# Kernel optimization log

Measured on AMD Instinct MI355X. Metric: run time of the kernel, lower is better.

The kernel has to match this reference:

```python
import jax, jax.numpy as jnp
import numpy as np

D, H, DK, L, F, V = 512, 16, 32, 16, 1024, 32768
C1, C2, CORE, LG, MD, B = 512, 256, 256, 64, 64, 16
T_IN = C1 + C2 + CORE      # 1024
T_TF = CORE + LG + MD      # 384


def _ln(x, g, b, eps=1e-5):
    mu = x.mean(-1, keepdims=True)
    var = ((x - mu) ** 2).mean(-1, keepdims=True)
    return (x - mu) * jax.lax.rsqrt(var + eps) * g + b


def _heads(x):  # [B,T,D] -> [B,H,T,DK]
    b, t, _ = x.shape
    return x.reshape(b, t, H, DK).transpose(0, 2, 1, 3)


def _summarizer(ids, sem, pos, inw, inb, outw, outb, tok, lng, lnb):
    b, t = ids.shape
    x = sem[ids] + pos[:t][None]                      # [B,T,D]
    wq, wk, wv = jnp.split(inw, 3, axis=0)
    bq, bk, bv = jnp.split(inb, 3, axis=0)
    q = _heads(jnp.broadcast_to(tok, (b, tok.shape[1], D)) @ wq.T + bq)
    k = _heads(x @ wk.T + bk)
    v = _heads(x @ wv.T + bv)
    s = jnp.einsum('bhqd,bhkd->bhqk', q, k) / jnp.sqrt(jnp.float32(DK))
    a = jax.nn.softmax(s, axis=-1)
    o = jnp.einsum('bhqk,bhkd->bhqd', a, v).transpose(0, 2, 1, 3).reshape(b, -1, D)
    return _ln(o @ outw.T + outb, lng, lnb)


def _forward(emb_sem, emb_pos,
             lg_sem, lg_pos, lg_inw, lg_inb, lg_outw, lg_outb, lg_tok, lg_lng, lg_lnb,
             md_sem, md_pos, md_inw, md_inb, md_outw, md_outb, md_tok, md_lng, md_lnb,
             qkv_w, qkv_b, wo_w, wo_b, ln1_g, ln1_b, ln2_g, ln2_b,
             ff1_w, ff1_b, ff2_w, ff2_b, hd_lng, hd_lnb, hd_w, hd_b,
             input_ids, target_ids):
    lg_ids = input_ids[:, -(C1 + C2 + CORE):-(C2 + CORE)]
    md_ids = input_ids[:, -(C2 + CORE):-CORE]
    core_ids = input_ids[:, -CORE:]
    tgt = target_ids[:, -CORE:]

    lg_emb = _summarizer(lg_ids, lg_sem, lg_pos, lg_inw, lg_inb, lg_outw, lg_outb, lg_tok, lg_lng, lg_lnb)
    md_emb = _summarizer(md_ids, md_sem, md_pos, md_inw, md_inb, md_outw, md_outb, md_tok, md_lng, md_lnb)
    x_core = emb_sem[core_ids] + emb_pos[:CORE][None]
    x = jnp.concatenate([lg_emb, md_emb, x_core], axis=1)   # [B, 384, D]

    mask = jnp.tril(jnp.ones((T_TF, T_TF), dtype=bool))

    def step(x, p):
        qw, qb, ow, ob, g1, b1, g2, b2, f1w, f1b, f2w, f2b = p
        h = _ln(x, g1, b1)
        qkv = h @ qw.T + qb
        q, k, v = (_heads(t) for t in jnp.split(qkv, 3, axis=-1))
        s = jnp.einsum('bhqd,bhkd->bhqk', q, k) / jnp.sqrt(jnp.float32(DK))
        s = jnp.where(mask, s, -jnp.inf)
        a = jax.nn.softmax(s, axis=-1)
        o = jnp.einsum('bhqk,bhkd->bhqd', a, v).transpose(0, 2, 1, 3).reshape(x.shape)
        x = x + o @ ow.T + ob
        h2 = _ln(x, g2, b2)
        ff = jax.nn.gelu(h2 @ f1w.T + f1b, approximate=False) @ f2w.T + f2b
        return x + ff, None

    x, _ = jax.lax.scan(step, x, (qkv_w, qkv_b, wo_w, wo_b, ln1_g, ln1_b,
                                  ln2_g, ln2_b, ff1_w, ff1_b, ff2_w, ff2_b))
    logits = (_ln(x, hd_lng, hd_lnb) @ hd_w.T + hd_b)[:, -CORE:, :]
    return logits, tgt


def setup_inputs() -> dict:
    key = jax.random.key(0)
    ks = jax.random.split(key, 24)
    def rn(k, shape, s=0.02):
        return jax.random.normal(k, shape, jnp.float32) * s
    z, o = jnp.zeros, jnp.ones
    return {
        'input_ids': jax.random.randint(ks[0], (B, T_IN), 0, V),
        'target_ids': jax.random.randint(ks[1], (B, T_IN), 0, V),
        'emb_sem': rn(ks[2], (V, D)), 'emb_pos': rn(ks[3], (CORE, D)),
        'lg_sem': rn(ks[4], (V, D)), 'lg_pos': rn(ks[5], (C1, D)),
        'lg_inw': rn(ks[6], (3 * D, D)), 'lg_inb': z(3 * D),
        'lg_outw': rn(ks[7], (D, D)), 'lg_outb': z(D),
        'lg_tok': rn(ks[8], (1, LG, D), 1.0), 'lg_lng': o(D), 'lg_lnb': z(D),
        'md_sem': rn(ks[9], (V, D)), 'md_pos': rn(ks[10], (C2, D)),
        'md_inw': rn(ks[11], (3 * D, D)), 'md_inb': z(3 * D),
        'md_outw': rn(ks[12], (D, D)), 'md_outb': z(D),
        'md_tok': rn(ks[13], (1, MD, D), 1.0), 'md_lng': o(D), 'md_lnb': z(D),
        'qkv_w': rn(ks[14], (L, 3 * D, D)), 'qkv_b': z((L, 3 * D)),
        'wo_w': rn(ks[15], (L, D, D)), 'wo_b': z((L, D)),
        'ln1_g': o((L, D)), 'ln1_b': z((L, D)), 'ln2_g': o((L, D)), 'ln2_b': z((L, D)),
        'ff1_w': rn(ks[16], (L, F, D)), 'ff1_b': z((L, F)),
        'ff2_w': rn(ks[17], (L, D, F)), 'ff2_b': z((L, D)),
        'hd_lng': o(D), 'hd_lnb': z(D), 'hd_w': rn(ks[18], (V, D)), 'hd_b': z(V),
    }


def reference(input_ids, target_ids, emb_sem, emb_pos,
              lg_sem, lg_pos, lg_inw, lg_inb, lg_outw, lg_outb, lg_tok, lg_lng, lg_lnb,
              md_sem, md_pos, md_inw, md_inb, md_outw, md_outb, md_tok, md_lng, md_lnb,
              qkv_w, qkv_b, wo_w, wo_b, ln1_g, ln1_b, ln2_g, ln2_b,
              ff1_w, ff1_b, ff2_w, ff2_b, hd_lng, hd_lnb, hd_w, hd_b):
    return _forward(emb_sem, emb_pos,
                    lg_sem, lg_pos, lg_inw, lg_inb, lg_outw, lg_outb, lg_tok, lg_lng, lg_lnb,
                    md_sem, md_pos, md_inw, md_inb, md_outw, md_outb, md_tok, md_lng, md_lnb,
                    qkv_w, qkv_b, wo_w, wo_b, ln1_g, ln1_b, ln2_g, ln2_b,
                    ff1_w, ff1_b, ff2_w, ff2_b, hd_lng, hd_lnb, hd_w, hd_b,
                    input_ids, target_ids)
```

## Files before the change

### kernel.cpp

```cpp
#include <hip/hip_runtime.h>
#include <hip/hip_bf16.h>
#include <math.h>

#define D 512
#define NHEAD 16
#define DK 32
#define NLAYER 16
#define FF 1024
#define VOC 32768
#define TTF 384
#define NCORE 256
#define NB 16

typedef __attribute__((ext_vector_type(8))) short bfrag;
typedef __attribute__((ext_vector_type(4))) float f32x4;

typedef __attribute__((address_space(3))) void lds_void;
typedef const __attribute__((address_space(1))) void gbl_void;
__device__ __forceinline__ void gload16(const void* g, void* l) {
    __builtin_amdgcn_global_load_lds((gbl_void*)g, (lds_void*)l, 16, 0, 0);
}

__device__ __forceinline__ float gelu_f(float v) {
    return 0.5f * v * (1.0f + erff(v * 0.70710678118654752f));
}

__device__ __forceinline__ void bf8_to_f32(uint4 u, float* v) {
    const __hip_bfloat16* t = reinterpret_cast<const __hip_bfloat16*>(&u);
    #pragma unroll
    for (int e = 0; e < 8; e++) v[e] = __bfloat162float(t[e]);
}
__device__ __forceinline__ uint4 f32_to_bf8(const float* v) {
    uint4 u; __hip_bfloat16* t = reinterpret_cast<__hip_bfloat16*>(&u);
    #pragma unroll
    for (int e = 0; e < 8; e++) t[e] = __float2bfloat16(v[e]);
    return u;
}

__global__ __launch_bounds__(256) void cvt_k(const float* __restrict__ in,
                                             __hip_bfloat16* __restrict__ out, int n)
{
    int i = (blockIdx.x * 256 + threadIdx.x) * 8;
    if (i >= n) return;
    float v[8];
    float4 a = *reinterpret_cast<const float4*>(in + i);
    float4 b = *reinterpret_cast<const float4*>(in + i + 4);
    v[0]=a.x; v[1]=a.y; v[2]=a.z; v[3]=a.w; v[4]=b.x; v[5]=b.y; v[6]=b.z; v[7]=b.w;
    *reinterpret_cast<uint4*>(out + i) = f32_to_bf8(v);
}

__global__ __launch_bounds__(256) void cvtpad_k(const float* __restrict__ in,
                                                __hip_bfloat16* __restrict__ out, int n, int ntot)
{
    int i = (blockIdx.x * 256 + threadIdx.x) * 8;
    if (i >= ntot) return;
    float v[8] = {0.f,0.f,0.f,0.f,0.f,0.f,0.f,0.f};
    if (i < n) {
        float4 a = *reinterpret_cast<const float4*>(in + i);
        float4 b = *reinterpret_cast<const float4*>(in + i + 4);
        v[0]=a.x; v[1]=a.y; v[2]=a.z; v[3]=a.w; v[4]=b.x; v[5]=b.y; v[6]=b.z; v[7]=b.w;
    }
    *reinterpret_cast<uint4*>(out + i) = f32_to_bf8(v);
}

__global__ __launch_bounds__(128) void embed_k(
    const int* __restrict__ ids, int id_stride, int id_off,
    const float* __restrict__ sem, const float* __restrict__ pos,
    __hip_bfloat16* __restrict__ out, int out_stride, int out_off)
{
    int t = blockIdx.x, b = blockIdx.y, tid = threadIdx.x;
    int id = ids[b * id_stride + id_off + t];
    const float4* s4 = reinterpret_cast<const float4*>(sem + (size_t)id * D);
    const float4* p4 = reinterpret_cast<const float4*>(pos + (size_t)t * D);
    size_t row = (size_t)(b * out_stride + out_off + t) * D;
    float4 a = s4[tid], p = p4[tid];
    __hip_bfloat16* o = out + row + tid * 4;
    o[0] = __float2bfloat16(a.x + p.x); o[1] = __float2bfloat16(a.y + p.y);
    o[2] = __float2bfloat16(a.z + p.z); o[3] = __float2bfloat16(a.w + p.w);
}

__global__ __launch_bounds__(256) void mgemm_k(
    const __hip_bfloat16* __restrict__ A, const __hip_bfloat16* __restrict__ W,
    const float* __restrict__ bias, void* __restrict__ C,
    int M, int N, int K, int flags, int order, int RT)
{
    __shared__ __align__(16) __hip_bfloat16 sA[2][8192];
    __shared__ __align__(16) __hip_bfloat16 sB[2][8192];
    int tid = threadIdx.x;
    int w = tid >> 6, lane = tid & 63;
    int wr = w >> 1, wc = w & 1;

    int nbx = gridDim.x, nby = gridDim.y;
    int nwg = nbx * nby;
    int bid0 = blockIdx.y * nbx + blockIdx.x;
    int bid = bid0;
    if (nwg >= 8) {
        int q = nwg >> 3, r = nwg & 7;
        int xcd = bid0 & 7, lb = bid0 >> 3;
        bid = (xcd < r ? xcd * (q + 1) : r * (q + 1) + (xcd - r) * q) + lb;
    }
    int bx, byg;
    if (order == 1) { bx = bid / nby; byg = bid - bx * nby; }
    else            { byg = bid / nbx; bx = bid - byg * nbx; }
    int col0 = bx * 128;

    int srow = lane >> 3;
    int scg  = (lane & 7) ^ srow;
    int cr = lane >> 4;
    int cc = lane & 15;

    const __hip_bfloat16* gB[4];
    #pragma unroll
    for (int r = 0; r < 4; r++) {
        int blk = r * 4 + w;
        gB[r] = W + (size_t)(col0 + blk * 8 + srow) * K + scg * 8;
    }

    for (int t = 0; t < RT; t++) {
        int row0 = (byg * RT + t) * 128;

        const __hip_bfloat16* gA[4];
        #pragma unroll
        for (int r = 0; r < 4; r++) {
            int blk = r * 4 + w;
            gA[r] = A + (size_t)(row0 + blk * 8 + srow) * K + scg * 8;
        }

        f32x4 acc[4][4];
        #pragma unroll
        for (int m = 0; m < 4; m++)
            #pragma unroll
            for (int n = 0; n < 4; n++) acc[m][n] = (f32x4){0.f, 0.f, 0.f, 0.f};

        auto stage = [&](int buf, int k0) {
            #pragma unroll
            for (int r = 0; r < 4; r++) {
                int blk = r * 4 + w;
                gload16(gA[r] + k0, &sA[buf][blk * 512]);
                gload16(gB[r] + k0, &sB[buf][blk * 512]);
            }
        };

        stage(0, 0);
        for (int k0 = 0; k0 < K; k0 += 64) {
            int p = (k0 >> 6) & 1;
            bool more = (k0 + 64 < K);
            if (more) {
                stage(p ^ 1, k0 + 64);
                asm volatile("s_waitcnt vmcnt(8)" ::: "memory");
            } else {
                asm volatile("s_waitcnt vmcnt(0)" ::: "memory");
            }
            __builtin_amdgcn_sched_barrier(0);
            __builtin_amdgcn_s_barrier();
            __builtin_amdgcn_sched_barrier(0);

            #pragma unroll
            for (int ks = 0; ks < 2; ks++) {
                bfrag af[4], bf[4];
                #pragma unroll
                for (int m = 0; m < 4; m++) {
                    int blk = wr * 8 + m * 2 + (cc >> 3);
                    int slot = (ks * 4 + cr) ^ (cc & 7);
                    af[m] = *reinterpret_cast<const bfrag*>(&sA[p][blk * 512 + (cc & 7) * 64 + slot * 8]);
                }
                #pragma unroll
                for (int n = 0; n < 4; n++) {
                    int blk = wc * 8 + n * 2 + (cc >> 3);
                    int slot = (ks * 4 + cr) ^ (cc & 7);
                    bf[n] = *reinterpret_cast<const bfrag*>(&sB[p][blk * 512 + (cc & 7) * 64 + slot * 8]);
                }
                #pragma unroll
                for (int m = 0; m < 4; m++)
                    #pragma unroll
                    for (int n = 0; n < 4; n++)
                        acc[m][n] = __builtin_amdgcn_mfma_f32_16x16x32_bf16(af[m], bf[n], acc[m][n], 0, 0, 0);
            }
            __builtin_amdgcn_sched_barrier(0);
            __builtin_amdgcn_s_barrier();
            __builtin_amdgcn_sched_barrier(0);
        }

        #pragma unroll
        for (int m = 0; m < 4; m++) {
            int rg = row0 + wr * 64 + m * 16 + cr * 4;
            #pragma unroll
            for (int n = 0; n < 4; n++) {
                int cg = col0 + wc * 64 + n * 16 + cc;
                float bs = bias[cg];
                #pragma unroll
                for (int j = 0; j < 4; j++) {
                    float v = acc[m][n][j] + bs;
                    size_t off = (size_t)(rg + j) * N + cg;
                    if (flags == 2)      ((__hip_bfloat16*)C)[off] = __float2bfloat16(gelu_f(v));
                    else if (flags == 3) ((__hip_bfloat16*)C)[off] = __float2bfloat16(v);
                    else                 ((float*)C)[off] = v;
                }
            }
        }
        if (t + 1 < RT) {
            __builtin_amdgcn_s_barrier();
        }
    }
}

template<int IB, int OB>
__global__ __launch_bounds__(256) void ln_k(
    const void* __restrict__ in, void* __restrict__ out,
    const float* __restrict__ g, const float* __restrict__ bt,
    int rpb, int in_stride, int in_off, int out_stride, int out_off)
{
    int r = blockIdx.x * 4 + (threadIdx.x >> 6);
    int b = r / rpb, t = r % rpb;
    size_t irow = (size_t)(b * in_stride + in_off + t) * D;
    size_t orow = (size_t)(b * out_stride + out_off + t) * D;
    int c0 = (threadIdx.x & 63) * 8;
    float v[8];
    if (IB) {
        bf8_to_f32(*reinterpret_cast<const uint4*>((const __hip_bfloat16*)in + irow + c0), v);
    } else {
        float4 a = *reinterpret_cast<const float4*>((const float*)in + irow + c0);
        float4 bq = *reinterpret_cast<const float4*>((const float*)in + irow + c0 + 4);
        v[0]=a.x; v[1]=a.y; v[2]=a.z; v[3]=a.w; v[4]=bq.x; v[5]=bq.y; v[6]=bq.z; v[7]=bq.w;
    }
    float s = 0.f;
    #pragma unroll
    for (int e = 0; e < 8; e++) s += v[e];
    #pragma unroll
    for (int off = 32; off; off >>= 1) s += __shfl_xor(s, off);
    float mu = s * (1.f / 512.f);
    float vs = 0.f;
    #pragma unroll
    for (int e = 0; e < 8; e++) { float d = v[e] - mu; vs += d * d; }
    #pragma unroll
    for (int off = 32; off; off >>= 1) vs += __shfl_xor(vs, off);
    float rstd = rsqrtf(vs * (1.f / 512.f) + 1e-5f);
    float y[8];
    #pragma unroll
    for (int e = 0; e < 8; e++) y[e] = (v[e] - mu) * rstd * g[c0 + e] + bt[c0 + e];
    if (OB) {
        *reinterpret_cast<uint4*>((__hip_bfloat16*)out + orow + c0) = f32_to_bf8(y);
    } else {
        *reinterpret_cast<float4*>((float*)out + orow + c0)     = make_float4(y[0], y[1], y[2], y[3]);
        *reinterpret_cast<float4*>((float*)out + orow + c0 + 4) = make_float4(y[4], y[5], y[6], y[7]);
    }
}

template<int WRITE_H>
__global__ __launch_bounds__(256) void res_ln_k(
    const __hip_bfloat16* __restrict__ delta, __hip_bfloat16* __restrict__ x,
    const float* __restrict__ g, const float* __restrict__ bt,
    __hip_bfloat16* __restrict__ h)
{
    int r = blockIdx.x * 4 + (threadIdx.x >> 6);
    int c0 = (threadIdx.x & 63) * 8;
    size_t row = (size_t)r * D + c0;
    float v[8], dv[8];
    bf8_to_f32(*reinterpret_cast<const uint4*>(x + row), v);
    bf8_to_f32(*reinterpret_cast<const uint4*>(delta + row), dv);
    #pragma unroll
    for (int e = 0; e < 8; e++) v[e] += dv[e];
    *reinterpret_cast<uint4*>(x + row) = f32_to_bf8(v);
    if (WRITE_H) {
        float s = 0.f;
        #pragma unroll
        for (int e = 0; e < 8; e++) s += v[e];
        #pragma unroll
        for (int off = 32; off; off >>= 1) s += __shfl_xor(s, off);
        float mu = s * (1.f / 512.f);
        float vs = 0.f;
        #pragma unroll
        for (int e = 0; e < 8; e++) { float d = v[e] - mu; vs += d * d; }
        #pragma unroll
        for (int off = 32; off; off >>= 1) vs += __shfl_xor(vs, off);
        float rstd = rsqrtf(vs * (1.f / 512.f) + 1e-5f);
        float y[8];
        #pragma unroll
        for (int e = 0; e < 8; e++) y[e] = (v[e] - mu) * rstd * g[c0 + e] + bt[c0 + e];
        *reinterpret_cast<uint4*>(h + row) = f32_to_bf8(y);
    }
}

__global__ __launch_bounds__(512) void fattn_k(
    const __hip_bfloat16* __restrict__ qkv, __hip_bfloat16* __restrict__ o)
{
    __shared__ __align__(16) __hip_bfloat16 Kl[24 * 512];
    __shared__ __align__(16) __hip_bfloat16 Vl[24 * 512];
    __shared__ __align__(16) __hip_bfloat16 Pl[8 * 512];
    int h = blockIdx.x, b = blockIdx.y;
    int tid = threadIdx.x, w = tid >> 6, l = tid & 63;
    const size_t base = (size_t)b * TTF * 1536 + h * DK;

    for (int it = 0; it < 3; it++) {
        int item = it * 512 + tid;
        int key = item >> 2, dg = item & 3;
        uint4 k4 = *reinterpret_cast<const uint4*>(qkv + base + (size_t)key * 1536 + 512 + dg * 8);
        *reinterpret_cast<uint4*>(&Kl[((key >> 4) * 64 + dg * 16 + (key & 15)) * 8]) = k4;
        uint4 v4 = *reinterpret_cast<const uint4*>(qkv + base + (size_t)key * 1536 + 1024 + dg * 8);
        const ushort* ve = reinterpret_cast<const ushort*>(&v4);
        #pragma unroll
        for (int e = 0; e < 8; e++) {
            int dk = dg * 8 + e;
            int f = (((key & 31) >> 3) << 4) | (dk & 15);
            int idx = (((key >> 5) << 1) + (dk >> 4)) * 512 + f * 8 + (key & 7);
            reinterpret_cast<ushort*>(Vl)[idx] = ve[e];
        }
    }
    __syncthreads();

    const float sc = 0.17677669529663687f;
    __hip_bfloat16* pw = Pl + w * 512;

    for (int iq = 0; iq < 3; iq++) {
        int qt = (iq == 0) ? w : (iq == 1 ? 15 - w : 16 + w);
        int q0 = qt * 16;
        bfrag qf = *reinterpret_cast<const bfrag*>(qkv + base + (size_t)(q0 + (l & 15)) * 1536 + (l >> 4) * 8);
        f32x4 oa0 = (f32x4){0.f, 0.f, 0.f, 0.f};
        f32x4 oa1 = (f32x4){0.f, 0.f, 0.f, 0.f};
        float mrun[4], lrun[4];
        #pragma unroll
        for (int jj = 0; jj < 4; jj++) { mrun[jj] = -3.0e38f; lrun[jj] = 0.f; }
        int ksmax = (q0 + 15) >> 5;

        for (int ks = 0; ks <= ksmax; ks++) {
            bfrag kf0 = *reinterpret_cast<const bfrag*>(&Kl[(ks * 2 + 0) * 512 + l * 8]);
            bfrag kf1 = *reinterpret_cast<const bfrag*>(&Kl[(ks * 2 + 1) * 512 + l * 8]);
            f32x4 z = (f32x4){0.f, 0.f, 0.f, 0.f};
            f32x4 s0 = __builtin_amdgcn_mfma_f32_16x16x32_bf16(qf, kf0, z, 0, 0, 0);
            f32x4 s1 = __builtin_amdgcn_mfma_f32_16x16x32_bf16(qf, kf1, z, 0, 0, 0);
            if (ks == ksmax) {
                #pragma unroll
                for (int jj = 0; jj < 4; jj++) {
                    int q = q0 + ((l >> 4) << 2) + jj;
                    if (ks * 32 + (l & 15) > q)      s0[jj] = -3.0e38f;
                    if (ks * 32 + 16 + (l & 15) > q) s1[jj] = -3.0e38f;
                }
            }
            float p0[4], p1[4], ps[4];
            #pragma unroll
            for (int jj = 0; jj < 4; jj++) {
                float sm = fmaxf(s0[jj], s1[jj]);
                #pragma unroll
                for (int off = 1; off <= 8; off <<= 1) sm = fmaxf(sm, __shfl_xor(sm, off));
                float mnew = fmaxf(mrun[jj], sm);
                float f = __expf((mrun[jj] - mnew) * sc);
                mrun[jj] = mnew;
                lrun[jj] *= f;
                oa0[jj] *= f; oa1[jj] *= f;
                p0[jj] = __expf((s0[jj] - mnew) * sc);
                p1[jj] = __expf((s1[jj] - mnew) * sc);
                ps[jj] = p0[jj] + p1[jj];
            }
            #pragma unroll
            for (int jj = 0; jj < 4; jj++) {
                float t = ps[jj];
                #pragma unroll
                for (int off = 1; off <= 8; off <<= 1) t += __shfl_xor(t, off);
                lrun[jj] += t;
            }
            #pragma unroll
            for (int jj = 0; jj < 4; jj++) {
                int ql = ((l >> 4) << 2) + jj;
                int kl0 = l & 15, kl1 = 16 + (l & 15);
                pw[((kl0 >> 3) * 16 + ql) * 8 + (kl0 & 7)] = __float2bfloat16(p0[jj]);
                pw[((kl1 >> 3) * 16 + ql) * 8 + (kl1 & 7)] = __float2bfloat16(p1[jj]);
            }
            bfrag pf  = *reinterpret_cast<const bfrag*>(&pw[l * 8]);
            bfrag vf0 = *reinterpret_cast<const bfrag*>(&Vl[(ks * 2 + 0) * 512 + l * 8]);
            bfrag vf1 = *reinterpret_cast<const bfrag*>(&Vl[(ks * 2 + 1) * 512 + l * 8]);
            oa0 = __builtin_amdgcn_mfma_f32_16x16x32_bf16(pf, vf0, oa0, 0, 0, 0);
            oa1 = __builtin_amdgcn_mfma_f32_16x16x32_bf16(pf, vf1, oa1, 0, 0, 0);
        }
        #pragma unroll
        for (int jj = 0; jj < 4; jj++) {
            float inv = 1.0f / lrun[jj];
            int q = q0 + ((l >> 4) << 2) + jj;
            size_t orow = ((size_t)b * TTF + q) * D + h * DK;
            o[orow + (l & 15)]      = __float2bfloat16(oa0[jj] * inv);
            o[orow + 16 + (l & 15)] = __float2bfloat16(oa1[jj] * inv);
        }
    }
}

template<int TLEN>
__global__ __launch_bounds__(256) void sattn_k(
    const __hip_bfloat16* __restrict__ q, const __hip_bfloat16* __restrict__ kv,
    __hip_bfloat16* __restrict__ o)
{
    __shared__ __align__(16) __hip_bfloat16 Kl[(TLEN / 16) * 512];
    __shared__ __align__(16) __hip_bfloat16 Vl[(TLEN / 16) * 512];
    __shared__ __align__(16) __hip_bfloat16 Pl[4 * 512];
    int h = blockIdx.x, b = blockIdx.y;
    int tid = threadIdx.x, w = tid >> 6, l = tid & 63;

    for (int it = 0; it < TLEN / 64; it++) {
        int item = it * 256 + tid;
        int key = item >> 2, dg = item & 3;
        const __hip_bfloat16* kr = kv + (size_t)(b * TLEN + key) * 1024 + h * DK + dg * 8;
        uint4 k4 = *reinterpret_cast<const uint4*>(kr);
        *reinterpret_cast<uint4*>(&Kl[((key >> 4) * 64 + dg * 16 + (key & 15)) * 8]) = k4;
        uint4 v4 = *reinterpret_cast<const uint4*>(kr + 512);
        const ushort* ve = reinterpret_cast<const ushort*>(&v4);
        #pragma unroll
        for (int e = 0; e < 8; e++) {
            int dk = dg * 8 + e;
            int f = (((key & 31) >> 3) << 4) | (dk & 15);
            int idx = (((key >> 5) << 1) + (dk >> 4)) * 512 + f * 8 + (key & 7);
            reinterpret_cast<ushort*>(Vl)[idx] = ve[e];
        }
    }
    __syncthreads();

    const float sc = 0.17677669529663687f;
    __hip_bfloat16* pw = Pl + w * 512;
    int q0 = w * 16;
    bfrag qf = *reinterpret_cast<const bfrag*>(q + (size_t)(q0 + (l & 15)) * D + h * DK + (l >> 4) * 8);
    f32x4 oa0 = (f32x4){0.f, 0.f, 0.f, 0.f};
    f32x4 oa1 = (f32x4){0.f, 0.f, 0.f, 0.f};
    float mrun[4], lrun[4];
    #pragma unroll
    for (int jj = 0; jj < 4; jj++) { mrun[jj] = -3.0e38f; lrun[jj] = 0.f; }

    for (int ks = 0; ks < TLEN / 32; ks++) {
        bfrag kf0 = *reinterpret_cast<const bfrag*>(&Kl[(ks * 2 + 0) * 512 + l * 8]);
        bfrag kf1 = *reinterpret_cast<const bfrag*>(&Kl[(ks * 2 + 1) * 512 + l * 8]);
        f32x4 z = (f32x4){0.f, 0.f, 0.f, 0.f};
        f32x4 s0 = __builtin_amdgcn_mfma_f32_16x16x32_bf16(qf, kf0, z, 0, 0, 0);
        f32x4 s1 = __builtin_amdgcn_mfma_f32_16x16x32_bf16(qf, kf1, z, 0, 0, 0);
        float p0[4], p1[4], ps[4];
        #pragma unroll
        for (int jj = 0; jj < 4; jj++) {
            float sm = fmaxf(s0[jj], s1[jj]);
            #pragma unroll
            for (int off = 1; off <= 8; off <<= 1) sm = fmaxf(sm, __shfl_xor(sm, off));
            float mnew = fmaxf(mrun[jj], sm);
            float f = __expf((mrun[jj] - mnew) * sc);
            mrun[jj] = mnew;
            lrun[jj] *= f;
            oa0[jj] *= f; oa1[jj] *= f;
            p0[jj] = __expf((s0[jj] - mnew) * sc);
            p1[jj] = __expf((s1[jj] - mnew) * sc);
            ps[jj] = p0[jj] + p1[jj];
        }
        #pragma unroll
        for (int jj = 0; jj < 4; jj++) {
            float t = ps[jj];
            #pragma unroll
            for (int off = 1; off <= 8; off <<= 1) t += __shfl_xor(t, off);
            lrun[jj] += t;
        }
        #pragma unroll
        for (int jj = 0; jj < 4; jj++) {
            int ql = ((l >> 4) << 2) + jj;
            int kl0 = l & 15, kl1 = 16 + (l & 15);
            pw[((kl0 >> 3) * 16 + ql) * 8 + (kl0 & 7)] = __float2bfloat16(p0[jj]);
            pw[((kl1 >> 3) * 16 + ql) * 8 + (kl1 & 7)] = __float2bfloat16(p1[jj]);
        }
        bfrag pf  = *reinterpret_cast<const bfrag*>(&pw[l * 8]);
        bfrag vf0 = *reinterpret_cast<const bfrag*>(&Vl[(ks * 2 + 0) * 512 + l * 8]);
        bfrag vf1 = *reinterpret_cast<const bfrag*>(&Vl[(ks * 2 + 1) * 512 + l * 8]);
        oa0 = __builtin_amdgcn_mfma_f32_16x16x32_bf16(pf, vf0, oa0, 0, 0, 0);
        oa1 = __builtin_amdgcn_mfma_f32_16x16x32_bf16(pf, vf1, oa1, 0, 0, 0);
    }
    #pragma unroll
    for (int jj = 0; jj < 4; jj++) {
        float inv = 1.0f / lrun[jj];
        int qi = q0 + ((l >> 4) << 2) + jj;
        size_t orow = ((size_t)b * 64 + qi) * D + h * DK;
        o[orow + (l & 15)]      = __float2bfloat16(oa0[jj] * inv);
        o[orow + 16 + (l & 15)] = __float2bfloat16(oa1[jj] * inv);
    }
}

__global__ __launch_bounds__(256) void tgt_k(const int* __restrict__ tids, float* __restrict__ out)
{
    int i = blockIdx.x * 256 + threadIdx.x;
    int b = i >> 8, c = i & 255;
    out[i] = (float)tids[b * 1024 + 768 + c];
}

extern "C" void kernel_launch(void* const* d_in, const int* in_sizes, int n_in,
                              void* d_out, int out_size, void* d_ws, size_t ws_size,
                              hipStream_t stream) {
    (void)in_sizes; (void)n_in; (void)out_size; (void)ws_size;
    const int*   input_ids  = (const int*)  d_in[0];
    const int*   target_ids = (const int*)  d_in[1];
    const float* emb_sem    = (const float*)d_in[2];
    const float* emb_pos    = (const float*)d_in[3];
    const float* lg_sem     = (const float*)d_in[4];
    const float* lg_pos     = (const float*)d_in[5];
    const float* lg_inw     = (const float*)d_in[6];
    const float* lg_inb     = (const float*)d_in[7];
    const float* lg_outw    = (const float*)d_in[8];
    const float* lg_outb    = (const float*)d_in[9];
    const float* lg_tok     = (const float*)d_in[10];
    const float* lg_lng     = (const float*)d_in[11];
    const float* lg_lnb     = (const float*)d_in[12];
    const float* md_sem     = (const float*)d_in[13];
    const float* md_pos     = (const float*)d_in[14];
    const float* md_inw     = (const float*)d_in[15];
    const float* md_inb     = (const float*)d_in[16];
    const float* md_outw    = (const float*)d_in[17];
    const float* md_outb    = (const float*)d_in[18];
    const float* md_tok     = (const float*)d_in[19];
    const float* md_lng     = (const float*)d_in[20];
    const float* md_lnb     = (const float*)d_in[21];
    const float* qkv_w      = (const float*)d_in[22];
    const float* qkv_b      = (const float*)d_in[23];
    const float* wo_w       = (const float*)d_in[24];
    const float* wo_b       = (const float*)d_in[25];
    const float* ln1_g      = (const float*)d_in[26];
    const float* ln1_b      = (const float*)d_in[27];
    const float* ln2_g      = (const float*)d_in[28];
    const float* ln2_b      = (const float*)d_in[29];
    const float* ff1_w      = (const float*)d_in[30];
    const float* ff1_b      = (const float*)d_in[31];
    const float* ff2_w      = (const float*)d_in[32];
    const float* ff2_b      = (const float*)d_in[33];
    const float* hd_lng     = (const float*)d_in[34];
    const float* hd_lnb     = (const float*)d_in[35];
    const float* hd_w       = (const float*)d_in[36];
    const float* hd_b       = (const float*)d_in[37];

    __hip_bfloat16* x_bf   = (__hip_bfloat16*)d_ws;
    __hip_bfloat16* h_bf   = x_bf   + 3145728;
    __hip_bfloat16* d_bf   = h_bf   + 3145728;
    __hip_bfloat16* a_bf   = d_bf   + 3145728;
    __hip_bfloat16* qkv_bf = a_bf   + 6291456;
    __hip_bfloat16* sumo_bf= qkv_bf + 9437184;
    __hip_bfloat16* w_qkv  = sumo_bf+ 524288;
    __hip_bfloat16* w_wo   = w_qkv  + 12582912;
    __hip_bfloat16* w_ff1  = w_wo   + 4194304;
    __hip_bfloat16* w_ff2  = w_ff1  + 8388608;
    __hip_bfloat16* w_hd   = w_ff2  + 8388608;
    __hip_bfloat16* w_lgin = w_hd   + 16777216;
    __hip_bfloat16* w_mdin = w_lgin + 786432;
    __hip_bfloat16* w_lgout= w_mdin + 786432;
    __hip_bfloat16* w_mdout= w_lgout+ 262144;
    __hip_bfloat16* tok_lg = w_mdout+ 262144;
    __hip_bfloat16* tok_md = tok_lg + 65536;
    __hip_bfloat16* q_bf   = tok_md + 65536;
    float* so2 = (float*)(q_bf + 65536);

    cvt_k<<<12582912 / 2048, 256, 0, stream>>>(qkv_w, w_qkv, 12582912);
    cvt_k<<< 4194304 / 2048, 256, 0, stream>>>(wo_w,  w_wo,   4194304);
    cvt_k<<< 8388608 / 2048, 256, 0, stream>>>(ff1_w, w_ff1,  8388608);
    cvt_k<<< 8388608 / 2048, 256, 0, stream>>>(ff2_w, w_ff2,  8388608);
    cvt_k<<<16777216 / 2048, 256, 0, stream>>>(hd_w,  w_hd,  16777216);
    cvt_k<<<  786432 / 2048, 256, 0, stream>>>(lg_inw, w_lgin, 786432);
    cvt_k<<<  786432 / 2048, 256, 0, stream>>>(md_inw, w_mdin, 786432);
    cvt_k<<<  262144 / 2048, 256, 0, stream>>>(lg_outw, w_lgout, 262144);
    cvt_k<<<  262144 / 2048, 256, 0, stream>>>(md_outw, w_mdout, 262144);
    cvtpad_k<<<32, 256, 0, stream>>>(lg_tok, tok_lg, 32768, 65536);
    cvtpad_k<<<32, 256, 0, stream>>>(md_tok, tok_md, 32768, 65536);

    embed_k<<<dim3(512, NB), 128, 0, stream>>>(input_ids, 1024, 0, lg_sem, lg_pos, a_bf, 512, 0);
    mgemm_k<<<dim3(8, 64), 256, 0, stream>>>(a_bf, w_lgin + 512 * 512, lg_inb + 512, qkv_bf, 8192, 1024, 512, 3, 0, 1);
    mgemm_k<<<dim3(4, 1), 256, 0, stream>>>(tok_lg, w_lgin, lg_inb, q_bf, 128, 512, 512, 3, 0, 1);
    sattn_k<512><<<dim3(NHEAD, NB), 256, 0, stream>>>(q_bf, qkv_bf, sumo_bf);
    mgemm_k<<<dim3(4, 8), 256, 0, stream>>>(sumo_bf, w_lgout, lg_outb, so2, 1024, 512, 512, 0, 0, 1);
    ln_k<0, 1><<<256, 256, 0, stream>>>(so2, x_bf, lg_lng, lg_lnb, 64, 64, 0, TTF, 0);

    embed_k<<<dim3(256, NB), 128, 0, stream>>>(input_ids, 1024, 512, md_sem, md_pos, a_bf, 256, 0);
    mgemm_k<<<dim3(8, 32), 256, 0, stream>>>(a_bf, w_mdin + 512 * 512, md_inb + 512, qkv_bf, 4096, 1024, 512, 3, 0, 1);
    mgemm_k<<<dim3(4, 1), 256, 0, stream>>>(tok_md, w_mdin, md_inb, q_bf, 128, 512, 512, 3, 0, 1);
    sattn_k<256><<<dim3(NHEAD, NB), 256, 0, stream>>>(q_bf, qkv_bf, sumo_bf);
    mgemm_k<<<dim3(4, 8), 256, 0, stream>>>(sumo_bf, w_mdout, md_outb, so2, 1024, 512, 512, 0, 0, 1);
    ln_k<0, 1><<<256, 256, 0, stream>>>(so2, x_bf, md_lng, md_lnb, 64, 64, 0, TTF, 64);

    embed_k<<<dim3(256, NB), 128, 0, stream>>>(input_ids, 1024, 768, emb_sem, emb_pos, x_bf, TTF, 128);

    ln_k<1, 1><<<1536, 256, 0, stream>>>(x_bf, h_bf, ln1_g, ln1_b, TTF, TTF, 0, TTF, 0);
    for (int l = 0; l < NLAYER; l++) {
        mgemm_k<<<dim3(12, 48), 256, 0, stream>>>(h_bf, w_qkv + (size_t)l * 1536 * 512, qkv_b + l * 1536, qkv_bf, 6144, 1536, 512, 3, 0, 1);
        fattn_k<<<dim3(NHEAD, NB), 512, 0, stream>>>(qkv_bf, a_bf);
        mgemm_k<<<dim3(4, 48), 256, 0, stream>>>(a_bf, w_wo + (size_t)l * 512 * 512, wo_b + l * D, d_bf, 6144, 512, 512, 3, 0, 1);
        res_ln_k<1><<<1536, 256, 0, stream>>>(d_bf, x_bf, ln2_g + l * D, ln2_b + l * D, h_bf);
        mgemm_k<<<dim3(8, 48), 256, 0, stream>>>(h_bf, w_ff1 + (size_t)l * 1024 * 512, ff1_b + l * FF, a_bf, 6144, 1024, 512, 2, 0, 1);
        mgemm_k<<<dim3(4, 48), 256, 0, stream>>>(a_bf, w_ff2 + (size_t)l * 512 * 1024, ff2_b + l * D, d_bf, 6144, 512, 1024, 3, 0, 1);
        if (l < NLAYER - 1) {
            res_ln_k<1><<<1536, 256, 0, stream>>>(d_bf, x_bf, ln1_g + (size_t)(l + 1) * D, ln1_b + (size_t)(l + 1) * D, h_bf);
        } else {
            res_ln_k<0><<<1536, 256, 0, stream>>>(d_bf, x_bf, hd_lng, hd_lnb, h_bf);
        }
    }

    ln_k<1, 1><<<1024, 256, 0, stream>>>(x_bf, h_bf, hd_lng, hd_lnb, NCORE, TTF, 128, NCORE, 0);
    float* logits = (float*)d_out;
    mgemm_k<<<dim3(256, 8), 256, 0, stream>>>(h_bf, w_hd, hd_b, logits, 4096, VOC, 512, 0, 1, 4);
    tgt_k<<<16, 256, 0, stream>>>(target_ids, logits + (size_t)NB * NCORE * VOC);
}
```

Baseline: 2.735 ms.

## Prefetch next row tile across tiles in GEMM, add MFMA priority in attention

The GEMM kernel now runs one flattened software pipeline across all row tiles, so the first K-slab of the next row tile is prefetched while the current tile finishes. This removes the pipeline drain and refill and the extra barrier between tiles. The attention kernels raise wave priority around their MFMA calls with s_setprio, and the head GEMM processes 8 row tiles per block over half as many blocks. Risks include less parallelism in the head GEMM, and a possible LDS buffer race because the epilogue no longer has a barrier before the prefetched stage overwrites the buffer.

After: 2.725 ms. About the same (-0.4%).

```diff
diff --git a/kernel.cpp b/kernel.cpp
--- a/kernel.cpp
+++ b/kernel.cpp
@@ -109,44 +109,37 @@
     int cr = lane >> 4;
     int cc = lane & 15;
 
-    const __hip_bfloat16* gB[4];
-    #pragma unroll
-    for (int r = 0; r < 4; r++) {
-        int blk = r * 4 + w;
-        gB[r] = W + (size_t)(col0 + blk * 8 + srow) * K + scg * 8;
-    }
-
+    auto stage = [&](int buf, int t, int k0) {
+        int r0 = (byg * RT + t) * 128;
+        #pragma unroll
+        for (int r = 0; r < 4; r++) {
+            int blk = r * 4 + w;
+            const __hip_bfloat16* pa = A + (size_t)(r0 + blk * 8 + srow) * K + scg * 8 + k0;
+            const __hip_bfloat16* pb = W + (size_t)(col0 + blk * 8 + srow) * K + scg * 8 + k0;
+            gload16(pa, &sA[buf][blk * 512]);
+            gload16(pb, &sB[buf][blk * 512]);
+        }
+    };
+
+    int ksteps = K >> 6;
+    int tsteps = RT * ksteps;
+
+    stage(0, 0, 0);
     for (int t = 0; t < RT; t++) {
         int row0 = (byg * RT + t) * 128;
 
-        const __hip_bfloat16* gA[4];
-        #pragma unroll
-        for (int r = 0; r < 4; r++) {
-            int blk = r * 4 + w;
-            gA[r] = A + (size_t)(row0 + blk * 8 + srow) * K + scg * 8;
-        }
-
         f32x4 acc[4][4];
         #pragma unroll
         for (int m = 0; m < 4; m++)
             #pragma unroll
             for (int n = 0; n < 4; n++) acc[m][n] = (f32x4){0.f, 0.f, 0.f, 0.f};
 
-        auto stage = [&](int buf, int k0) {
-            #pragma unroll
-            for (int r = 0; r < 4; r++) {
-                int blk = r * 4 + w;
-                gload16(gA[r] + k0, &sA[buf][blk * 512]);
-                gload16(gB[r] + k0, &sB[buf][blk * 512]);
-            }
-        };
-
-        stage(0, 0);
-        for (int k0 = 0; k0 < K; k0 += 64) {
-            int p = (k0 >> 6) & 1;
-            bool more = (k0 + 64 < K);
-            if (more) {
-                stage(p ^ 1, k0 + 64);
+        for (int kk = 0; kk < ksteps; kk++) {
+            int s = t * ksteps + kk;
+            int p = s & 1;
+            if (s + 1 < tsteps) {
+                int ns = s + 1;
+                stage(p ^ 1, ns / ksteps, (ns % ksteps) << 6);
                 asm volatile("s_waitcnt vmcnt(8)" ::: "memory");
             } else {
                 asm volatile("s_waitcnt vmcnt(0)" ::: "memory");
@@ -197,9 +190,6 @@
                     else                 ((float*)C)[off] = v;
                 }
             }
-        }
-        if (t + 1 < RT) {
-            __builtin_amdgcn_s_barrier();
         }
     }
 }
@@ -326,8 +316,10 @@
             bfrag kf0 = *reinterpret_cast<const bfrag*>(&Kl[(ks * 2 + 0) * 512 + l * 8]);
             bfrag kf1 = *reinterpret_cast<const bfrag*>(&Kl[(ks * 2 + 1) * 512 + l * 8]);
             f32x4 z = (f32x4){0.f, 0.f, 0.f, 0.f};
+            __builtin_amdgcn_s_setprio(1);
             f32x4 s0 = __builtin_amdgcn_mfma_f32_16x16x32_bf16(qf, kf0, z, 0, 0, 0);
             f32x4 s1 = __builtin_amdgcn_mfma_f32_16x16x32_bf16(qf, kf1, z, 0, 0, 0);
+            __builtin_amdgcn_s_setprio(0);
             if (ks == ksmax) {
                 #pragma unroll
                 for (int jj = 0; jj < 4; jj++) {
@@ -368,8 +360,10 @@
             bfrag pf  = *reinterpret_cast<const bfrag*>(&pw[l * 8]);
             bfrag vf0 = *reinterpret_cast<const bfrag*>(&Vl[(ks * 2 + 0) * 512 + l * 8]);
             bfrag vf1 = *reinterpret_cast<const bfrag*>(&Vl[(ks * 2 + 1) * 512 + l * 8]);
+            __builtin_amdgcn_s_setprio(1);
             oa0 = __builtin_amdgcn_mfma_f32_16x16x32_bf16(pf, vf0, oa0, 0, 0, 0);
             oa1 = __builtin_amdgcn_mfma_f32_16x16x32_bf16(pf, vf1, oa1, 0, 0, 0);
+            __builtin_amdgcn_s_setprio(0);
         }
         #pragma unroll
         for (int jj = 0; jj < 4; jj++) {
@@ -425,8 +419,10 @@
         bfrag kf0 = *reinterpret_cast<const bfrag*>(&Kl[(ks * 2 + 0) * 512 + l * 8]);
         bfrag kf1 = *reinterpret_cast<const bfrag*>(&Kl[(ks * 2 + 1) * 512 + l * 8]);
         f32x4 z = (f32x4){0.f, 0.f, 0.f, 0.f};
+        __builtin_amdgcn_s_setprio(1);
         f32x4 s0 = __builtin_amdgcn_mfma_f32_16x16x32_bf16(qf, kf0, z, 0, 0, 0);
         f32x4 s1 = __builtin_amdgcn_mfma_f32_16x16x32_bf16(qf, kf1, z, 0, 0, 0);
+        __builtin_amdgcn_s_setprio(0);
         float p0[4], p1[4], ps[4];
         #pragma unroll
         for (int jj = 0; jj < 4; jj++) {
@@ -459,8 +455,10 @@
         bfrag pf  = *reinterpret_cast<const bfrag*>(&pw[l * 8]);
         bfrag vf0 = *reinterpret_cast<const bfrag*>(&Vl[(ks * 2 + 0) * 512 + l * 8]);
         bfrag vf1 = *reinterpret_cast<const bfrag*>(&Vl[(ks * 2 + 1) * 512 + l * 8]);
+        __builtin_amdgcn_s_setprio(1);
         oa0 = __builtin_amdgcn_mfma_f32_16x16x32_bf16(pf, vf0, oa0, 0, 0, 0);
         oa1 = __builtin_amdgcn_mfma_f32_16x16x32_bf16(pf, vf1, oa1, 0, 0, 0);
+        __builtin_amdgcn_s_setprio(0);
     }
     #pragma unroll
     for (int jj = 0; jj < 4; jj++) {
@@ -587,6 +585,6 @@
 
     ln_k<1, 1><<<1024, 256, 0, stream>>>(x_bf, h_bf, hd_lng, hd_lnb, NCORE, TTF, 128, NCORE, 0);
     float* logits = (float*)d_out;
-    mgemm_k<<<dim3(256, 8), 256, 0, stream>>>(h_bf, w_hd, hd_b, logits, 4096, VOC, 512, 0, 1, 4);
+    mgemm_k<<<dim3(256, 4), 256, 0, stream>>>(h_bf, w_hd, hd_b, logits, 4096, VOC, 512, 0, 1, 8);
     tgt_k<<<16, 256, 0, stream>>>(target_ids, logits + (size_t)NB * NCORE * VOC);
 }
```
